# Optimization experiments

Hardware: AMD Instinct MI355X
Metric: run time of the kernel (lower is better)

The kernel has to match this reference:

```python
import jax, jax.numpy as jnp
import numpy as np

CUTOFF = 5.0
NUM_RBF = 8
POLY_P = 5
AVG_NEIGH = 16.0
NUM_LAYERS = 2
NUM_RANKS = 4  # edge angular ranks 0..3 (Cartesian dims 1,3,9,27)
C = 64


def _radial(edge_vec):
    # r: [E,1]; Bessel-j0 basis with polynomial cutoff envelope (MACE-style)
    r = jnp.sqrt(jnp.sum(edge_vec * edge_vec, axis=-1, keepdims=True) + 1e-12)
    x = r / CUTOFF
    p = float(POLY_P)
    env = (1.0 - 0.5 * (p + 1.0) * (p + 2.0) * x**POLY_P
           + p * (p + 2.0) * x**(POLY_P + 1)
           - 0.5 * p * (p + 1.0) * x**(POLY_P + 2))
    env = jnp.where(x < 1.0, env, 0.0)
    k = jnp.arange(1, NUM_RBF + 1, dtype=edge_vec.dtype)
    basis = jnp.sqrt(2.0 / CUTOFF) * jnp.sin(k * jnp.pi * x) / r  # [E,K]
    return basis * env, r


def _angular(rhat):
    # Cartesian ICTD-style angular basis, ranks 0..3, norm constants sqrt(2r+1)
    E = rhat.shape[0]
    y0 = jnp.ones((E, 1), rhat.dtype)
    y1 = jnp.sqrt(3.0) * rhat  # [E,3]
    o2 = rhat[:, :, None] * rhat[:, None, :]
    y2 = jnp.sqrt(5.0) * o2.reshape(E, 9)
    o3 = o2[:, :, :, None] * rhat[:, None, None, :]
    y3 = jnp.sqrt(7.0) * o3.reshape(E, 27)
    return (y0, y1, y2, y3)


def setup_inputs() -> dict:
    key = jax.random.key(0)
    ks = jax.random.split(key, 12)
    N, E = 5000, 80000
    species = jax.random.randint(ks[0], (N,), 0, 10, dtype=jnp.int32)
    senders = jax.random.randint(ks[1], (E,), 0, N, dtype=jnp.int32)
    receivers = jax.random.randint(ks[2], (E,), 0, N, dtype=jnp.int32)
    edge_vec = 1.5 * jax.random.normal(ks[3], (E, 3), jnp.float32)
    embed_w = jax.random.normal(ks[4], (10, C), jnp.float32)
    rad_w1 = jax.random.normal(ks[5], (NUM_LAYERS, NUM_RBF, 64), jnp.float32) / np.sqrt(NUM_RBF)
    rad_w2 = jax.random.normal(ks[6], (NUM_LAYERS, 64, 64), jnp.float32) / 8.0
    rad_w3 = jax.random.normal(ks[7], (NUM_LAYERS, 64, 64), jnp.float32) / 8.0
    rad_w4 = jax.random.normal(ks[8], (NUM_LAYERS, 64, NUM_RANKS * C), jnp.float32) / 8.0
    mix_w = jax.random.normal(ks[9], (NUM_LAYERS, NUM_RANKS, C, C), jnp.float32) / 8.0
    read_w = jax.random.normal(ks[10], (NUM_LAYERS, C), jnp.float32) / 8.0
    return {"species": species, "senders": senders, "receivers": receivers,
            "edge_vec": edge_vec, "embed_w": embed_w, "rad_w1": rad_w1,
            "rad_w2": rad_w2, "rad_w3": rad_w3, "rad_w4": rad_w4,
            "mix_w": mix_w, "read_w": read_w}


def reference(species, senders, receivers, edge_vec, embed_w,
              rad_w1, rad_w2, rad_w3, rad_w4, mix_w, read_w):
    N = species.shape[0]
    E = edge_vec.shape[0]
    rb, r = _radial(edge_vec)                      # [E,K]
    rhat = edge_vec / r
    Y = _angular(rhat)                             # tuple of [E,dim_r]
    h0 = embed_w[species]                          # [N,C] species embedding
    node_energy = jnp.zeros((N,), edge_vec.dtype)
    for l in range(NUM_LAYERS):
        # radial MLP -> per-rank, per-channel edge weights [E, NUM_RANKS, C]
        h = jax.nn.silu(rb @ rad_w1[l])
        h = jax.nn.silu(h @ rad_w2[l])
        h = jax.nn.silu(h @ rad_w3[l])
        R = (h @ rad_w4[l]).reshape(E, NUM_RANKS, C)
        hj = h0[senders]                           # neighbor gather [E,C]
        h0_new = jnp.zeros_like(h0)
        for ri in range(NUM_RANKS):
            # equivariant edge tensor product: radial * scalar feat x angular
            m = (R[:, ri, :] * hj)[:, :, None] * Y[ri][:, None, :]  # [E,C,dim]
            A = jax.ops.segment_sum(m, receivers, num_segments=N) / AVG_NEIGH
            if ri == 0:
                h0_new = h0_new + A[..., 0] @ mix_w[l, 0]
            else:
                # correlation-2 invariant contraction of equivariant features
                h0_new = h0_new + jnp.einsum('ncd,ncd->nc', A, A) @ mix_w[l, ri]
        node_energy = node_energy + h0_new @ read_w[l]
        h0 = h0_new
    return node_energy
```

## Files before the change

### kernel.cpp

```cpp
#include <hip/hip_runtime.h>
#include <math.h>


#define PI_F 3.14159265358979323846f
#define LOG2E_F 1.44269504088896340736f

typedef _Float16 f16x8 __attribute__((ext_vector_type(8)));
typedef float f32x4 __attribute__((ext_vector_type(4)));

union FU { uint4 u; f16x8 h; };

__device__ __forceinline__ float silu_f(float x) {
    float e = __builtin_amdgcn_exp2f(-LOG2E_F * x);
    return x * __builtin_amdgcn_rcpf(1.0f + e);
}

__device__ __forceinline__ uint pack2_f16(float a, float b) {
    return __builtin_bit_cast(uint, __builtin_amdgcn_cvt_pkrtz(a, b));
}

__device__ __forceinline__ float unpk_f16(uint u, int hi) {
    unsigned short s = hi ? (unsigned short)(u >> 16) : (unsigned short)(u & 0xffff);
    return (float)__builtin_bit_cast(_Float16, s);
}

__global__ void k_setup(const float* __restrict__ rw1,
                        const float* __restrict__ rw2,
                        const float* __restrict__ rw3,
                        const float* __restrict__ rw4,
                        uint* __restrict__ Wf1, uint* __restrict__ Wf2,
                        uint* __restrict__ Wf3, uint* __restrict__ Wf4,
                        const int* __restrict__ species,
                        const float* __restrict__ embw,
                        float* __restrict__ h0,
                        int* __restrict__ counts, int* __restrict__ cursor,
                        int N, int NC)
{
    int tid = blockIdx.x * blockDim.x + threadIdx.x;
    if (tid < N) { counts[tid] = 0; cursor[tid] = 0; }
    if (tid < NC) {
        int n = tid >> 6, c = tid & 63;
        h0[tid] = embw[species[n]*64 + c];
    }
    if (tid < 2048) {
        int reg = tid & 3, lane = (tid >> 2) & 63, ot = (tid >> 8) & 3, l = tid >> 10;
        int out = 16*ot + (lane & 15);
        int k   = 8*(lane >> 4) + 2*reg;
        float lo = (k   < 8) ? rw1[l*512 + k*64 + out]     : 0.0f;
        float hi = (k+1 < 8) ? rw1[l*512 + (k+1)*64 + out] : 0.0f;
        Wf1[tid] = pack2_f16(lo, hi);
    }
    if (tid >= 2048 && tid < 2048 + 4096) {
        int t = tid - 2048;
        int reg = t & 3, lane = (t >> 2) & 63, kt = (t >> 8) & 1, ot = (t >> 9) & 3, l = t >> 11;
        int out = 16*ot + (lane & 15);
        int k   = 32*kt + 8*(lane >> 4) + 2*reg;
        Wf2[t] = pack2_f16(rw2[l*4096 + k*64 + out], rw2[l*4096 + (k+1)*64 + out]);
    }
    if (tid >= 6144 && tid < 6144 + 4096) {
        int t = tid - 6144;
        int reg = t & 3, lane = (t >> 2) & 63, kt = (t >> 8) & 1, ot = (t >> 9) & 3, l = t >> 11;
        int out = 16*ot + (lane & 15);
        int k   = 32*kt + 8*(lane >> 4) + 2*reg;
        Wf3[t] = pack2_f16(rw3[l*4096 + k*64 + out], rw3[l*4096 + (k+1)*64 + out]);
    }
    if (tid >= 10240 && tid < 10240 + 16384) {
        int t = tid - 10240;
        int reg = t & 3, lane = (t >> 2) & 63, kt = (t >> 8) & 1, ot = (t >> 9) & 15, l = t >> 13;
        int out = 16*ot + (lane & 15);
        int k   = 32*kt + 8*(lane >> 4) + 2*reg;
        Wf4[t] = pack2_f16(rw4[l*16384 + k*256 + out], rw4[l*16384 + (k+1)*256 + out]);
    }
}

__global__ void k_edge_basis(const float* __restrict__ ev,
                             const int* __restrict__ recv,
                             uint*  __restrict__ rbh,
                             float* __restrict__ rhat4,
                             int*   __restrict__ counts,
                             int E)
{
    int e = blockIdx.x * blockDim.x + threadIdx.x;
    if (e >= E) return;
    float vx = ev[3*e+0], vy = ev[3*e+1], vz = ev[3*e+2];
    float r2 = vx*vx + vy*vy + vz*vz + 1e-12f;
    float r  = sqrtf(r2);
    float x  = r * 0.2f;
    float x2 = x*x;
    float x5 = x2*x2*x;
    float env = 1.0f + x5*(-21.0f + x*(35.0f - 15.0f*x));
    if (x >= 1.0f) env = 0.0f;
    float pref = 0.632455532033675866f / r * env;
    float pix  = PI_F * x;
    float bas[8];
    #pragma unroll
    for (int k = 0; k < 8; ++k) bas[k] = pref * __sinf((float)(k+1) * pix);
    uint* o = rbh + (size_t)e*4;
    #pragma unroll
    for (int k = 0; k < 4; ++k) o[k] = pack2_f16(bas[2*k], bas[2*k+1]);

    float ir = 1.0f / r;
    float4 rh;
    rh.x = vx*ir; rh.y = vy*ir; rh.z = vz*ir; rh.w = 0.0f;
    *(float4*)(rhat4 + (size_t)e*4) = rh;

    atomicAdd(&counts[recv[e]], 1);
}

__global__ void k_scan(const int* __restrict__ counts, int* __restrict__ offsets, int N)
{
    __shared__ int wsum[16];
    __shared__ int basev;
    int lane = threadIdx.x & 63;
    int w    = threadIdx.x >> 6;
    if (threadIdx.x == 0) basev = 0;
    __syncthreads();
    for (int start = 0; start < N; start += 1024) {
        int i = start + (int)threadIdx.x;
        int v = (i < N) ? counts[i] : 0;
        int s = v;
        #pragma unroll
        for (int off = 1; off < 64; off <<= 1) {
            int t = __shfl_up(s, off, 64);
            if (lane >= off) s += t;
        }
        if (lane == 63) wsum[w] = s;
        __syncthreads();
        int wbase = 0;
        {
            int ws = (lane < 16) ? wsum[lane] : 0;
            #pragma unroll
            for (int off = 1; off < 16; off <<= 1) {
                int t = __shfl_up(ws, off, 64);
                if (lane >= off) ws += t;
            }
            int excl = __shfl(ws, w - 1, 64);
            wbase = (w == 0) ? 0 : excl;
        }
        if (i < N) offsets[i] = basev + wbase + s - v;
        __syncthreads();
        if (threadIdx.x == 1023) basev += wbase + s;
        __syncthreads();
    }
    if (threadIdx.x == 0) offsets[N] = basev;
}

__global__ void k_scatter(const int* __restrict__ recv,
                          const int* __restrict__ offsets,
                          int* __restrict__ cursor,
                          int* __restrict__ elist, int E)
{
    int e = blockIdx.x * blockDim.x + threadIdx.x;
    if (e >= E) return;
    int r = recv[e];
    int p = atomicAdd(&cursor[r], 1);
    elist[offsets[r] + p] = e;
}

__global__ __launch_bounds__(256) void k_sort_wave(
    const int* __restrict__ offsets, int* __restrict__ elist, int N)
{
    int lane = threadIdx.x & 63;
    int node = (blockIdx.x * blockDim.x + threadIdx.x) >> 6;
    if (node >= N) return;
    int beg = offsets[node], end = offsets[node+1];
    int d = end - beg;
    if (d <= 1) return;
    if (d <= 64) {
        int v = (lane < d) ? elist[beg + lane] : 0x7fffffff;
        int rank = 0;
        #pragma unroll 8
        for (int j = 0; j < 64; ++j) {
            int vj = __shfl(v, j, 64);
            rank += (vj < v) ? 1 : 0;
        }
        if (lane < d) elist[beg + rank] = v;
    } else {
        if (lane == 0) {
            for (int i = beg + 1; i < end; ++i) {
                int v = elist[i];
                int j = i - 1;
                while (j >= beg && elist[j] > v) { elist[j+1] = elist[j]; --j; }
                elist[j+1] = v;
            }
        }
    }
}

__global__ __launch_bounds__(256) void k_mlp_mfma(
    const uint* __restrict__ rbh,
    const uint* __restrict__ Wf1, const uint* __restrict__ Wf2,
    const uint* __restrict__ Wf3, const uint* __restrict__ Wf4,
    uint* __restrict__ Rpk,
    int E, int tiles)
{
    __shared__ __align__(16) uint Hl[4][16][132];
    int lane = threadIdx.x & 63;
    int w    = threadIdx.x >> 6;
    int wid  = blockIdx.x * 4 + w;
    if (wid >= 2 * tiles) return;
    int l    = wid / tiles;
    int tile = wid % tiles;
    int e0   = tile * 16;

    uint (*H)[132] = Hl[w];
    int er = lane & 15;
    int kb = lane >> 4;

    f32x4 zero4 = {0.f, 0.f, 0.f, 0.f};

    FU b;
    if (kb == 0) {
        int e = e0 + er;
        if (e < E) b.u = *(const uint4*)(rbh + (size_t)e*4);
        else       b.u = make_uint4(0,0,0,0);
    } else {
        b.u = make_uint4(0,0,0,0);
    }
    f32x4 d[4];
    #pragma unroll
    for (int ot = 0; ot < 4; ++ot) {
        FU a;
        a.u = *(const uint4*)(Wf1 + ((size_t)(l*4 + ot)*64 + lane)*4);
        d[ot] = __builtin_amdgcn_mfma_f32_16x16x32_f16(a.h, b.h, zero4, 0, 0, 0);
    }
    #pragma unroll
    for (int ot = 0; ot < 4; ++ot) {
        uint p0 = pack2_f16(silu_f(d[ot][0]), silu_f(d[ot][1]));
        uint p1 = pack2_f16(silu_f(d[ot][2]), silu_f(d[ot][3]));
        uint* dst = &H[er][8*ot + 2*kb];
        dst[0] = p0; dst[1] = p1;
    }

    const uint* Wfs[2] = { Wf2, Wf3 };
    #pragma unroll
    for (int s = 0; s < 2; ++s) {
        FU hb0, hb1;
        hb0.u = *(const uint4*)&H[er][4*kb];
        hb1.u = *(const uint4*)&H[er][16 + 4*kb];
        #pragma unroll
        for (int ot = 0; ot < 4; ++ot) {
            FU a;
            a.u = *(const uint4*)(Wfs[s] + ((size_t)((l*4 + ot)*2 + 0)*64 + lane)*4);
            d[ot] = __builtin_amdgcn_mfma_f32_16x16x32_f16(a.h, hb0.h, zero4, 0, 0, 0);
            a.u = *(const uint4*)(Wfs[s] + ((size_t)((l*4 + ot)*2 + 1)*64 + lane)*4);
            d[ot] = __builtin_amdgcn_mfma_f32_16x16x32_f16(a.h, hb1.h, d[ot], 0, 0, 0);
        }
        #pragma unroll
        for (int ot = 0; ot < 4; ++ot) {
            uint p0 = pack2_f16(silu_f(d[ot][0]), silu_f(d[ot][1]));
            uint p1 = pack2_f16(silu_f(d[ot][2]), silu_f(d[ot][3]));
            uint* dst = &H[er][8*ot + 2*kb];
            dst[0] = p0; dst[1] = p1;
        }
    }

    FU hb0, hb1;
    hb0.u = *(const uint4*)&H[er][4*kb];
    hb1.u = *(const uint4*)&H[er][16 + 4*kb];
    #pragma unroll
    for (int ri = 0; ri < 4; ++ri) {
        #pragma unroll
        for (int otl = 0; otl < 4; ++otl) {
            int ot = ri*4 + otl;
            FU a;
            f32x4 d2;
            a.u = *(const uint4*)(Wf4 + ((size_t)((l*16 + ot)*2 + 0)*64 + lane)*4);
            d2 = __builtin_amdgcn_mfma_f32_16x16x32_f16(a.h, hb0.h, zero4, 0, 0, 0);
            a.u = *(const uint4*)(Wf4 + ((size_t)((l*16 + ot)*2 + 1)*64 + lane)*4);
            d2 = __builtin_amdgcn_mfma_f32_16x16x32_f16(a.h, hb1.h, d2, 0, 0, 0);
            int p = otl*8 + kb*2;
            H[er][(p  )*4 + ri] = pack2_f16(d2[0], d2[1]);
            H[er][(p+1)*4 + ri] = pack2_f16(d2[2], d2[3]);
        }
    }
    #pragma unroll
    for (int it = 0; it < 8; ++it) {
        int f   = it*64 + lane;
        int row = f >> 5;
        int q4  = (f & 31) * 4;
        int eg  = e0 + row;
        if (eg < E)
            *(uint4*)(Rpk + ((size_t)l*E + eg)*128 + q4) = *(const uint4*)&H[row][q4];
    }
}

__global__ __launch_bounds__(256) void k_node(
    const uint*  __restrict__ Rpk,
    const float* __restrict__ h0,
    const int*   __restrict__ senders,
    const float* __restrict__ rhat4,
    const int*   __restrict__ offsets,
    const int*   __restrict__ elist,
    const float* __restrict__ mixw,
    const float* __restrict__ readw,
    float* __restrict__ h0n,
    const float* __restrict__ eprev,
    float* __restrict__ eout,
    int N)
{
    int gtid = blockIdx.x * blockDim.x + threadIdx.x;
    int wave = gtid >> 6;
    int lane = threadIdx.x & 63;
    int w    = threadIdx.x >> 6;
    __shared__ float Bl[4][4][64];
    bool active = (wave < N);
    int n = active ? wave : 0;
    int half  = lane & 1;
    int cpair = lane >> 1;

    float a0 = 0.f;
    float a1[3]  = {0.f,0.f,0.f};
    float a2[6]  = {0.f,0.f,0.f,0.f,0.f,0.f};
    float a3[10] = {0.f,0.f,0.f,0.f,0.f,0.f,0.f,0.f,0.f,0.f};

    auto accum = [&](float x, float y, float z, float hj, uint4 qv) {
        float t0 = unpk_f16(qv.x, half) * hj;
        float t1 = unpk_f16(qv.y, half) * hj;
        float t2 = unpk_f16(qv.z, half) * hj;
        float t3 = unpk_f16(qv.w, half) * hj;
        a0 += t0;
        a1[0] = fmaf(t1, x, a1[0]);
        a1[1] = fmaf(t1, y, a1[1]);
        a1[2] = fmaf(t1, z, a1[2]);
        float qxx = x*x, qxy = x*y, qxz = x*z, qyy = y*y, qyz = y*z, qzz = z*z;
        a2[0] = fmaf(t2, qxx, a2[0]);
        a2[1] = fmaf(t2, qxy, a2[1]);
        a2[2] = fmaf(t2, qxz, a2[2]);
        a2[3] = fmaf(t2, qyy, a2[3]);
        a2[4] = fmaf(t2, qyz, a2[4]);
        a2[5] = fmaf(t2, qzz, a2[5]);
        float u0 = t3*qxx, u1 = t3*qxy, u3 = t3*qyy, u5 = t3*qzz;
        a3[0] = fmaf(u0, x, a3[0]);
        a3[1] = fmaf(u0, y, a3[1]);
        a3[2] = fmaf(u0, z, a3[2]);
        a3[3] = fmaf(u3, x, a3[3]);
        a3[4] = fmaf(u1, z, a3[4]);
        a3[5] = fmaf(u5, x, a3[5]);
        a3[6] = fmaf(u3, y, a3[6]);
        a3[7] = fmaf(u3, z, a3[7]);
        a3[8] = fmaf(u5, y, a3[8]);
        a3[9] = fmaf(u5, z, a3[9]);
    };

    if (active) {
        int beg = __builtin_amdgcn_readfirstlane(offsets[n]);
        int end = __builtin_amdgcn_readfirstlane(offsets[n+1]);
        int i = beg;
        int nfull = (end - beg) >> 2;

        int eA[4], snA[4]; float4 rhA[4]; float hjA[4]; uint4 qA[4];
        int eB[4], snB[4]; float4 rhB[4]; float hjB[4]; uint4 qB[4];

        auto loadb = [&](int ii, int (&e_)[4], int (&sn_)[4],
                         float4 (&rh_)[4], float (&hj_)[4], uint4 (&q_)[4]) {
            #pragma unroll
            for (int k = 0; k < 4; ++k) {
                e_[k]  = __builtin_amdgcn_readfirstlane(elist[ii+k]);
                sn_[k] = __builtin_amdgcn_readfirstlane(senders[e_[k]]);
            }
            #pragma unroll
            for (int k = 0; k < 4; ++k) {
                rh_[k] = *(const float4*)(rhat4 + (size_t)e_[k]*4);
                hj_[k] = h0[(size_t)sn_[k]*64 + lane];
                q_[k]  = *(const uint4*)(Rpk + (size_t)e_[k]*128 + cpair*4);
            }
        };
        auto accumb = [&](float4 (&rh_)[4], float (&hj_)[4], uint4 (&q_)[4]) {
            #pragma unroll
            for (int k = 0; k < 4; ++k)
                accum(rh_[k].x, rh_[k].y, rh_[k].z, hj_[k], q_[k]);
        };

        if (nfull > 0) {
            loadb(i, eA, snA, rhA, hjA, qA);
            int b = 0;
            for (;;) {
                if (b + 1 < nfull) {
                    loadb(i + 4, eB, snB, rhB, hjB, qB);
                    accumb(rhA, hjA, qA);
                    ++b; i += 4;
                    if (b + 1 < nfull) {
                        loadb(i + 4, eA, snA, rhA, hjA, qA);
                        accumb(rhB, hjB, qB);
                        ++b; i += 4;
                    } else {
                        accumb(rhB, hjB, qB);
                        ++b; i += 4;
                        break;
                    }
                } else {
                    accumb(rhA, hjA, qA);
                    ++b; i += 4;
                    break;
                }
            }
        }
        for (; i < end; ++i) {
            int e   = __builtin_amdgcn_readfirstlane(elist[i]);
            int snd = __builtin_amdgcn_readfirstlane(senders[e]);
            float4 rh = *(const float4*)(rhat4 + (size_t)e*4);
            float  hj = h0[(size_t)snd*64 + lane];
            uint4  qv = *(const uint4*)(Rpk + (size_t)e*128 + cpair*4);
            accum(rh.x, rh.y, rh.z, hj, qv);
        }
    }

    float B0 = a0 * 0.0625f;
    float s1 = a1[0]*a1[0] + a1[1]*a1[1] + a1[2]*a1[2];
    float B1 = s1 * (3.0f/256.0f);
    float s2 = a2[0]*a2[0] + a2[3]*a2[3] + a2[5]*a2[5]
             + 2.0f*(a2[1]*a2[1] + a2[2]*a2[2] + a2[4]*a2[4]);
    float B2 = s2 * (5.0f/256.0f);
    float s3 = a3[0]*a3[0] + a3[6]*a3[6] + a3[9]*a3[9]
             + 3.0f*(a3[1]*a3[1] + a3[2]*a3[2] + a3[3]*a3[3]
                   + a3[5]*a3[5] + a3[7]*a3[7] + a3[8]*a3[8])
             + 6.0f*a3[4]*a3[4];
    float B3 = s3 * (7.0f/256.0f);

    Bl[w][0][lane] = B0;
    Bl[w][1][lane] = B1;
    Bl[w][2][lane] = B2;
    Bl[w][3][lane] = B3;
    __syncthreads();

    if (active) {
        float acc = 0.0f;
        for (int ri = 0; ri < 4; ++ri) {
            #pragma unroll 8
            for (int j = 0; j < 64; ++j)
                acc = fmaf(Bl[w][ri][j], mixw[(ri*64 + j)*64 + lane], acc);
        }
        h0n[(size_t)n*64 + lane] = acc;

        float evl = acc * readw[lane];
        #pragma unroll
        for (int off = 1; off < 64; off <<= 1) evl += __shfl_xor(evl, off, 64);
        if (lane == 0) {
            float o = evl;
            if (eprev) o += eprev[n];
            eout[n] = o;
        }
    }
}

extern "C" void kernel_launch(void* const* d_in, const int* in_sizes, int n_in,
                              void* d_out, int out_size, void* d_ws, size_t ws_size,
                              hipStream_t stream)
{
    const int*   species   = (const int*)  d_in[0];
    const int*   senders   = (const int*)  d_in[1];
    const int*   receivers = (const int*)  d_in[2];
    const float* edge_vec  = (const float*)d_in[3];
    const float* embed_w   = (const float*)d_in[4];
    const float* rad_w1    = (const float*)d_in[5];
    const float* rad_w2    = (const float*)d_in[6];
    const float* rad_w3    = (const float*)d_in[7];
    const float* rad_w4    = (const float*)d_in[8];
    const float* mix_w     = (const float*)d_in[9];
    const float* read_w    = (const float*)d_in[10];

    int N = in_sizes[0];
    int E = in_sizes[1];
    float* out = (float*)d_out;

    char* ws = (char*)d_ws;
    size_t off = 0;
    auto alloc = [&](size_t bytes) -> char* {
        char* p = ws + off;
        off = (off + bytes + 255) & ~(size_t)255;
        return p;
    };
    uint*  rbh   = (uint*) alloc((size_t)E*4*sizeof(uint));
    float* rhat4 = (float*)alloc((size_t)E*4*sizeof(float));
    float* h0a   = (float*)alloc((size_t)N*64*sizeof(float));
    float* h0b   = (float*)alloc((size_t)N*64*sizeof(float));
    float* ener  = (float*)alloc((size_t)N*sizeof(float));
    int* counts  = (int*)alloc((size_t)N*sizeof(int));
    int* offsets = (int*)alloc((size_t)(N+1)*sizeof(int));
    int* cursor  = (int*)alloc((size_t)N*sizeof(int));
    int* elist   = (int*)alloc((size_t)E*sizeof(int));
    uint* Wf1    = (uint*)alloc(2048*sizeof(uint));
    uint* Wf2    = (uint*)alloc(4096*sizeof(uint));
    uint* Wf3    = (uint*)alloc(4096*sizeof(uint));
    uint* Wf4    = (uint*)alloc(16384*sizeof(uint));
    uint* Rpk    = (uint*)alloc((size_t)2*E*128*sizeof(uint));

    int NC = N * 64;
    k_setup<<<(NC + 255)/256, 256, 0, stream>>>(
        rad_w1, rad_w2, rad_w3, rad_w4, Wf1, Wf2, Wf3, Wf4,
        species, embed_w, h0a, counts, cursor, N, NC);

    k_edge_basis<<<(E + 255)/256, 256, 0, stream>>>(
        edge_vec, receivers, rbh, rhat4, counts, E);
    k_scan<<<1, 1024, 0, stream>>>(counts, offsets, N);
    k_scatter<<<(E + 255)/256, 256, 0, stream>>>(receivers, offsets, cursor, elist, E);
    k_sort_wave<<<((size_t)N*64 + 255)/256, 256, 0, stream>>>(offsets, elist, N);

    int tiles = (E + 15) / 16;
    int waves = 2 * tiles;
    k_mlp_mfma<<<(waves + 3)/4, 256, 0, stream>>>(
        rbh, Wf1, Wf2, Wf3, Wf4, Rpk, E, tiles);

    float* hcur = h0a;
    float* hnxt = h0b;
    for (int l = 0; l < 2; ++l) {
        uint* Rl = Rpk + (size_t)l * E * 128;
        k_node<<<((size_t)N*64 + 255)/256, 256, 0, stream>>>(
            Rl, hcur, senders, rhat4, offsets, elist,
            mix_w + (size_t)l*4*64*64,
            read_w + (size_t)l*64,
            hnxt,
            (l == 0) ? nullptr : ener,
            (l == 0) ? ener : out,
            N);
        float* tmp = hcur; hcur = hnxt; hnxt = tmp;
    }
}
```

Baseline: 128.0 us.

## Store edge data in receiver-sorted CSR order to remove indirection in node kernel

Adds a permute kernel that writes sender indices and rhat into receiver-sorted slot order and builds an edge-to-slot map. The MLP kernel scatters its per-edge radial outputs directly into those sorted slots, so the node kernel reads Rpk, rhat and senders contiguously without the elist/senders dependent-load chain. The node loop is also simplified from a manual double-buffered prefetch to a plain unrolled 4-edge loop. This costs an extra launch, scattered writes in the MLP kernel and loss of explicit software prefetching.

```diff
diff --git a/kernel.cpp b/kernel.cpp
--- a/kernel.cpp
+++ b/kernel.cpp
@@ -187,10 +187,27 @@
     }
 }
 
+__global__ void k_permute(const int* __restrict__ elist,
+                          const int* __restrict__ senders,
+                          const float* __restrict__ rhat4,
+                          int* __restrict__ eslot,
+                          int* __restrict__ csr_send,
+                          float* __restrict__ csr_rhat,
+                          int E)
+{
+    int s = blockIdx.x * blockDim.x + threadIdx.x;
+    if (s >= E) return;
+    int e = elist[s];
+    eslot[e] = s;
+    csr_send[s] = senders[e];
+    *(float4*)(csr_rhat + (size_t)s*4) = *(const float4*)(rhat4 + (size_t)e*4);
+}
+
 __global__ __launch_bounds__(256) void k_mlp_mfma(
     const uint* __restrict__ rbh,
     const uint* __restrict__ Wf1, const uint* __restrict__ Wf2,
     const uint* __restrict__ Wf3, const uint* __restrict__ Wf4,
+    const int* __restrict__ eslot,
     uint* __restrict__ Rpk,
     int E, int tiles)
 {
@@ -280,18 +297,19 @@
         int row = f >> 5;
         int q4  = (f & 31) * 4;
         int eg  = e0 + row;
-        if (eg < E)
-            *(uint4*)(Rpk + ((size_t)l*E + eg)*128 + q4) = *(const uint4*)&H[row][q4];
+        if (eg < E) {
+            int slot = eslot[eg];
+            *(uint4*)(Rpk + ((size_t)l*E + slot)*128 + q4) = *(const uint4*)&H[row][q4];
+        }
     }
 }
 
 __global__ __launch_bounds__(256) void k_node(
     const uint*  __restrict__ Rpk,
     const float* __restrict__ h0,
-    const int*   __restrict__ senders,
-    const float* __restrict__ rhat4,
+    const int*   __restrict__ csr_send,
+    const float* __restrict__ csr_rhat,
     const int*   __restrict__ offsets,
-    const int*   __restrict__ elist,
     const float* __restrict__ mixw,
     const float* __restrict__ readw,
     float* __restrict__ h0n,
@@ -347,61 +365,26 @@
         int beg = __builtin_amdgcn_readfirstlane(offsets[n]);
         int end = __builtin_amdgcn_readfirstlane(offsets[n+1]);
         int i = beg;
-        int nfull = (end - beg) >> 2;
-
-        int eA[4], snA[4]; float4 rhA[4]; float hjA[4]; uint4 qA[4];
-        int eB[4], snB[4]; float4 rhB[4]; float hjB[4]; uint4 qB[4];
-
-        auto loadb = [&](int ii, int (&e_)[4], int (&sn_)[4],
-                         float4 (&rh_)[4], float (&hj_)[4], uint4 (&q_)[4]) {
+        for (; i + 4 <= end; i += 4) {
+            int sn_[4]; float4 rh_[4]; float hj_[4]; uint4 q_[4];
+            #pragma unroll
+            for (int k = 0; k < 4; ++k) sn_[k] = csr_send[i+k];
             #pragma unroll
             for (int k = 0; k < 4; ++k) {
-                e_[k]  = __builtin_amdgcn_readfirstlane(elist[ii+k]);
-                sn_[k] = __builtin_amdgcn_readfirstlane(senders[e_[k]]);
+                rh_[k] = *(const float4*)(csr_rhat + (size_t)(i+k)*4);
+                q_[k]  = *(const uint4*)(Rpk + (size_t)(i+k)*128 + cpair*4);
             }
             #pragma unroll
-            for (int k = 0; k < 4; ++k) {
-                rh_[k] = *(const float4*)(rhat4 + (size_t)e_[k]*4);
-                hj_[k] = h0[(size_t)sn_[k]*64 + lane];
-                q_[k]  = *(const uint4*)(Rpk + (size_t)e_[k]*128 + cpair*4);
-            }
-        };
-        auto accumb = [&](float4 (&rh_)[4], float (&hj_)[4], uint4 (&q_)[4]) {
+            for (int k = 0; k < 4; ++k) hj_[k] = h0[(size_t)sn_[k]*64 + lane];
             #pragma unroll
             for (int k = 0; k < 4; ++k)
                 accum(rh_[k].x, rh_[k].y, rh_[k].z, hj_[k], q_[k]);
-        };
-
-        if (nfull > 0) {
-            loadb(i, eA, snA, rhA, hjA, qA);
-            int b = 0;
-            for (;;) {
-                if (b + 1 < nfull) {
-                    loadb(i + 4, eB, snB, rhB, hjB, qB);
-                    accumb(rhA, hjA, qA);
-                    ++b; i += 4;
-                    if (b + 1 < nfull) {
-                        loadb(i + 4, eA, snA, rhA, hjA, qA);
-                        accumb(rhB, hjB, qB);
-                        ++b; i += 4;
-                    } else {
-                        accumb(rhB, hjB, qB);
-                        ++b; i += 4;
-                        break;
-                    }
-                } else {
-                    accumb(rhA, hjA, qA);
-                    ++b; i += 4;
-                    break;
-                }
-            }
         }
         for (; i < end; ++i) {
-            int e   = __builtin_amdgcn_readfirstlane(elist[i]);
-            int snd = __builtin_amdgcn_readfirstlane(senders[e]);
-            float4 rh = *(const float4*)(rhat4 + (size_t)e*4);
+            int snd = csr_send[i];
+            float4 rh = *(const float4*)(csr_rhat + (size_t)i*4);
+            uint4  qv = *(const uint4*)(Rpk + (size_t)i*128 + cpair*4);
             float  hj = h0[(size_t)snd*64 + lane];
-            uint4  qv = *(const uint4*)(Rpk + (size_t)e*128 + cpair*4);
             accum(rh.x, rh.y, rh.z, hj, qv);
         }
     }
@@ -471,20 +454,23 @@
         off = (off + bytes + 255) & ~(size_t)255;
         return p;
     };
-    uint*  rbh   = (uint*) alloc((size_t)E*4*sizeof(uint));
-    float* rhat4 = (float*)alloc((size_t)E*4*sizeof(float));
-    float* h0a   = (float*)alloc((size_t)N*64*sizeof(float));
-    float* h0b   = (float*)alloc((size_t)N*64*sizeof(float));
-    float* ener  = (float*)alloc((size_t)N*sizeof(float));
-    int* counts  = (int*)alloc((size_t)N*sizeof(int));
-    int* offsets = (int*)alloc((size_t)(N+1)*sizeof(int));
-    int* cursor  = (int*)alloc((size_t)N*sizeof(int));
-    int* elist   = (int*)alloc((size_t)E*sizeof(int));
-    uint* Wf1    = (uint*)alloc(2048*sizeof(uint));
-    uint* Wf2    = (uint*)alloc(4096*sizeof(uint));
-    uint* Wf3    = (uint*)alloc(4096*sizeof(uint));
-    uint* Wf4    = (uint*)alloc(16384*sizeof(uint));
-    uint* Rpk    = (uint*)alloc((size_t)2*E*128*sizeof(uint));
+    uint*  rbh     = (uint*) alloc((size_t)E*4*sizeof(uint));
+    float* rhat4   = (float*)alloc((size_t)E*4*sizeof(float));
+    float* h0a     = (float*)alloc((size_t)N*64*sizeof(float));
+    float* h0b     = (float*)alloc((size_t)N*64*sizeof(float));
+    float* ener    = (float*)alloc((size_t)N*sizeof(float));
+    int* counts    = (int*)alloc((size_t)N*sizeof(int));
+    int* offsets   = (int*)alloc((size_t)(N+1)*sizeof(int));
+    int* cursor    = (int*)alloc((size_t)N*sizeof(int));
+    int* elist     = (int*)alloc((size_t)E*sizeof(int));
+    int* eslot     = (int*)alloc((size_t)E*sizeof(int));
+    int* csr_send  = (int*)alloc((size_t)E*sizeof(int));
+    float* csr_rhat= (float*)alloc((size_t)E*4*sizeof(float));
+    uint* Wf1      = (uint*)alloc(2048*sizeof(uint));
+    uint* Wf2      = (uint*)alloc(4096*sizeof(uint));
+    uint* Wf3      = (uint*)alloc(4096*sizeof(uint));
+    uint* Wf4      = (uint*)alloc(16384*sizeof(uint));
+    uint* Rpk      = (uint*)alloc((size_t)2*E*128*sizeof(uint));
 
     int NC = N * 64;
     k_setup<<<(NC + 255)/256, 256, 0, stream>>>(
@@ -496,18 +482,20 @@
     k_scan<<<1, 1024, 0, stream>>>(counts, offsets, N);
     k_scatter<<<(E + 255)/256, 256, 0, stream>>>(receivers, offsets, cursor, elist, E);
     k_sort_wave<<<((size_t)N*64 + 255)/256, 256, 0, stream>>>(offsets, elist, N);
+    k_permute<<<(E + 255)/256, 256, 0, stream>>>(
+        elist, senders, rhat4, eslot, csr_send, csr_rhat, E);
 
     int tiles = (E + 15) / 16;
     int waves = 2 * tiles;
     k_mlp_mfma<<<(waves + 3)/4, 256, 0, stream>>>(
-        rbh, Wf1, Wf2, Wf3, Wf4, Rpk, E, tiles);
+        rbh, Wf1, Wf2, Wf3, Wf4, eslot, Rpk, E, tiles);
 
     float* hcur = h0a;
     float* hnxt = h0b;
     for (int l = 0; l < 2; ++l) {
         uint* Rl = Rpk + (size_t)l * E * 128;
         k_node<<<((size_t)N*64 + 255)/256, 256, 0, stream>>>(
-            Rl, hcur, senders, rhat4, offsets, elist,
+            Rl, hcur, csr_send, csr_rhat, offsets,
             mix_w + (size_t)l*4*64*64,
             read_w + (size_t)l*64,
             hnxt,
```

After: 113.1 us. 1.13x faster.
